# Kernel tuning notes

Measured on AMD Instinct MI355X. Metric: run time of the kernel, lower is better.

The kernel has to match this reference:

```python
import jax, jax.numpy as jnp
import numpy as np

EPS = 1e-5

def layer_norm(x, g, b):
    m = x.mean(-1, keepdims=True)
    v = ((x - m) ** 2).mean(-1, keepdims=True)
    return (x - m) * jax.lax.rsqrt(v + EPS) * g + b

def setup_inputs() -> dict:
    key = jax.random.key(0)
    ks = jax.random.split(key, 8)
    H, T = 512, 256
    hidden_states = jax.random.normal(ks[0], (1, T, H), jnp.float32)
    U = jax.random.normal(ks[1], (H, H), jnp.float32) * 0.01
    W = jax.random.normal(ks[2], (H, H), jnp.float32) * 0.01
    a = jax.random.normal(ks[3], (H,), jnp.float32) * 0.01
    b = jax.random.normal(ks[4], (H,), jnp.float32) * 0.01
    gamma = jnp.ones((H,), jnp.float32)
    beta = jnp.zeros((H,), jnp.float32)
    targets = jax.random.randint(ks[5], (T,), 0, H)  # deterministic stand-in for torch.randint dummy targets
    return {"hidden_states": hidden_states, "U": U, "W": W, "a": a, "b": b,
            "gamma": gamma, "beta": beta, "targets": targets}

def reference(hidden_states, U, W, a, b, gamma, beta, targets):
    # batch must be 1 (torch.outer in the original requires 1-D vectors)
    h = hidden_states[0]                      # (T, H)
    z = jax.nn.relu(h @ U + a)                # (T, H) slow-path hidden

    # Per-timestep grads of CE(LayerNorm(z_t @ W + b), target_t) w.r.t. W, b
    def step_loss(z_t, tgt, W_, b_):
        y = layer_norm(z_t @ W_ + b_, gamma, beta)
        return -jax.nn.log_softmax(y)[tgt]
    grad_fn = jax.grad(step_loss, argnums=(2, 3))
    gradW, gradb = jax.vmap(grad_fn, in_axes=(0, 0, None, None))(z, targets, W, b)  # (T,H,H), (T,H)

    # W_update_t[p,q] = sum_{i<t} h_i[p] * h_t[q] * gradW_i[p,q]
    G = h[:, :, None] * gradW                 # (T, H, H)
    A = jnp.cumsum(G, axis=0) - G             # exclusive prefix sum over i
    W_upd = A * h[:, None, :]                 # (T, H, H)
    fastW = W - jnp.cumsum(W_upd, axis=0)     # cumulative fast weights per t

    # b_update_t[q] = h_t[q] * sum_{i<t} (sum_p h_i[p]) * gradb_i[q]
    c = h.sum(-1)                             # (T,)
    Bc = c[:, None] * gradb                   # (T, H)
    Bex = jnp.cumsum(Bc, axis=0) - Bc         # exclusive
    b_upd = h * Bex
    fastb = b - jnp.cumsum(b_upd, axis=0)     # (T, H)

    pre = jnp.einsum('th,thq->tq', z, fastW) + fastb
    out = layer_norm(pre, gamma, beta)        # (T, H)
    return out[None]                          # (1, T, H)
```

## Files before the change

### kernel.cpp

```cpp
#include <hip/hip_runtime.h>

#define T 256
#define H 512
#define EPSF 1e-5f

__device__ __forceinline__ float block_sum(float v, float* s4) {
    for (int o = 32; o; o >>= 1) v += __shfl_xor(v, o);
    int w = threadIdx.x >> 6;
    __syncthreads();
    if ((threadIdx.x & 63) == 0) s4[w] = v;
    __syncthreads();
    return s4[0] + s4[1] + s4[2] + s4[3];
}

__device__ __forceinline__ float block_max(float v, float* s4) {
    for (int o = 32; o; o >>= 1) v = fmaxf(v, __shfl_xor(v, o));
    int w = threadIdx.x >> 6;
    __syncthreads();
    if ((threadIdx.x & 63) == 0) s4[w] = v;
    __syncthreads();
    return fmaxf(fmaxf(s4[0], s4[1]), fmaxf(s4[2], s4[3]));
}

__global__ __launch_bounds__(256) void k1(
        const float* __restrict__ h, const float* __restrict__ U,
        const float* __restrict__ a, float* __restrict__ Z,
        float* __restrict__ HZ, float* __restrict__ c, float* __restrict__ S) {
    int bid = blockIdx.x, tid = threadIdx.x;
    int lane = tid & 63, w = tid >> 6;
    if (bid < 8) {
        __shared__ float csum[4][64];
        int q = bid * 64 + lane;
        int tbase = w * 64;
        float s = 0.f;
        for (int j = 0; j < 64; j += 8) {
            float v[8];
            #pragma unroll
            for (int u = 0; u < 8; ++u) v[u] = h[(tbase + j + u) * H + q];
            #pragma unroll
            for (int u = 0; u < 8; ++u) s += v[u];
        }
        csum[w][lane] = s;
        __syncthreads();
        float acc = 0.f;
        #pragma unroll
        for (int w2 = 0; w2 < 3; ++w2) if (w2 < w) acc += csum[w2][lane];
        for (int j = 0; j < 64; j += 8) {
            float v[8];
            #pragma unroll
            for (int u = 0; u < 8; ++u) v[u] = h[(tbase + j + u) * H + q];
            #pragma unroll
            for (int u = 0; u < 8; ++u) { acc += v[u]; S[(tbase + j + u) * H + q] = acc; }
        }
        return;
    }
    int b = bid - 8;
    int t0 = (b >> 2) * 2, qt = b & 3;
    __shared__ __align__(16) float sh[1024];
    __shared__ float2 part[3][2][64];
    ((float4*)sh)[tid] = ((const float4*)(h + t0 * H))[tid];
    __syncthreads();

    if (qt == 0 && w < 2) {
        float s = 0.f;
        #pragma unroll
        for (int j = 0; j < 8; ++j) s += sh[w * 512 + lane + j * 64];
        for (int o = 32; o; o >>= 1) s += __shfl_xor(s, o);
        if (lane == 0) c[t0 + w] = s;
    }

    int qc = qt * 64 + lane;
    const float2* U2 = (const float2*)U;
    float2 acc0 = {0.f, 0.f}, acc1 = {0.f, 0.f};
    int kbeg = w * 128;
    for (int k0 = kbeg; k0 < kbeg + 128; k0 += 8) {
        float2 bv[8];
        #pragma unroll
        for (int u = 0; u < 8; ++u) bv[u] = U2[(k0 + u) * 256 + qc];
        float a0[8], a1[8];
        #pragma unroll
        for (int u = 0; u < 8; ++u) { a0[u] = sh[k0 + u]; a1[u] = sh[512 + k0 + u]; }
        #pragma unroll
        for (int u = 0; u < 8; ++u) {
            acc0.x += a0[u] * bv[u].x; acc0.y += a0[u] * bv[u].y;
            acc1.x += a1[u] * bv[u].x; acc1.y += a1[u] * bv[u].y;
        }
    }
    if (w) { part[w - 1][0][lane] = acc0; part[w - 1][1][lane] = acc1; }
    __syncthreads();
    if (w == 0) {
        #pragma unroll
        for (int p = 0; p < 3; ++p) {
            acc0.x += part[p][0][lane].x; acc0.y += part[p][0][lane].y;
            acc1.x += part[p][1][lane].x; acc1.y += part[p][1][lane].y;
        }
        float2 av = ((const float2*)a)[qc];
        float z0x = fmaxf(acc0.x + av.x, 0.f), z0y = fmaxf(acc0.y + av.y, 0.f);
        float z1x = fmaxf(acc1.x + av.x, 0.f), z1y = fmaxf(acc1.y + av.y, 0.f);
        float2 h0 = ((float2*)sh)[qc], h1 = ((float2*)sh)[256 + qc];
        ((float2*)Z)[t0 * 256 + qc]        = make_float2(z0x, z0y);
        ((float2*)Z)[(t0 + 1) * 256 + qc]  = make_float2(z1x, z1y);
        ((float2*)HZ)[t0 * 256 + qc]       = make_float2(h0.x * z0x, h0.y * z0y);
        ((float2*)HZ)[(t0 + 1) * 256 + qc] = make_float2(h1.x * z1x, h1.y * z1y);
    }
}

__global__ __launch_bounds__(256) void k2(
        const float* __restrict__ Z, const float* __restrict__ W,
        const float* __restrict__ bb, const float* __restrict__ HZ,
        const float* __restrict__ c, float* __restrict__ u0,
        float* __restrict__ Beta) {
    __shared__ __align__(16) float smem[2 * 8 * 516 + 256];
    int bid = blockIdx.x, tid = threadIdx.x;
    int lane = tid & 63, w = tid >> 6;
    if (bid < 512) {
        float* sh = smem;
        float2* part = (float2*)(smem + 1024);
        int t0 = (bid >> 2) * 2, qt = bid & 3;
        ((float4*)sh)[tid] = ((const float4*)(Z + t0 * H))[tid];
        __syncthreads();
        int qc = qt * 64 + lane;
        const float2* W2 = (const float2*)W;
        float2 acc0 = {0.f, 0.f}, acc1 = {0.f, 0.f};
        int kbeg = w * 128;
        for (int k0 = kbeg; k0 < kbeg + 128; k0 += 8) {
            float2 bv[8];
            #pragma unroll
            for (int u = 0; u < 8; ++u) bv[u] = W2[(k0 + u) * 256 + qc];
            float a0[8], a1[8];
            #pragma unroll
            for (int u = 0; u < 8; ++u) { a0[u] = sh[k0 + u]; a1[u] = sh[512 + k0 + u]; }
            #pragma unroll
            for (int u = 0; u < 8; ++u) {
                acc0.x += a0[u] * bv[u].x; acc0.y += a0[u] * bv[u].y;
                acc1.x += a1[u] * bv[u].x; acc1.y += a1[u] * bv[u].y;
            }
        }
        if (w) { part[((w - 1) * 2 + 0) * 64 + lane] = acc0; part[((w - 1) * 2 + 1) * 64 + lane] = acc1; }
        __syncthreads();
        if (w == 0) {
            #pragma unroll
            for (int p = 0; p < 3; ++p) {
                float2 p0 = part[(p * 2 + 0) * 64 + lane];
                float2 p1 = part[(p * 2 + 1) * 64 + lane];
                acc0.x += p0.x; acc0.y += p0.y;
                acc1.x += p1.x; acc1.y += p1.y;
            }
            float2 bv = ((const float2*)bb)[qc];
            ((float2*)u0)[t0 * 256 + qc]       = make_float2(acc0.x + bv.x, acc0.y + bv.y);
            ((float2*)u0)[(t0 + 1) * 256 + qc] = make_float2(acc1.x + bv.x, acc1.y + bv.y);
        }
    } else {
        int b = bid - 512;
        int ti = b >> 5, ii = b & 31;
        if (ii > ti) return;
        int t0 = ti * 8, i0 = ii * 8;
        float* Zs = smem;
        float* Hs = smem + 8 * 516;
        float* red = smem + 2 * 8 * 516;
        #pragma unroll
        for (int j = 0; j < 4; ++j) {
            int idx = tid + j * 256;
            int row = idx >> 7, col4 = idx & 127;
            float4 v = ((const float4*)(Z + (t0 + row) * H))[col4];
            *(float4*)&Zs[row * 516 + col4 * 4] = v;
            float4 g = ((const float4*)(HZ + (i0 + row) * H))[col4];
            *(float4*)&Hs[row * 516 + col4 * 4] = g;
        }
        __syncthreads();
        int ks = tid >> 6, r = (tid >> 3) & 7, ci = tid & 7;
        float acc = 0.f;
        int kb = ks * 128;
        #pragma unroll 4
        for (int k0 = kb; k0 < kb + 128; k0 += 8) {
            float4 z0 = *(float4*)&Zs[r * 516 + k0];
            float4 z1 = *(float4*)&Zs[r * 516 + k0 + 4];
            float4 h0 = *(float4*)&Hs[ci * 516 + k0];
            float4 h1 = *(float4*)&Hs[ci * 516 + k0 + 4];
            acc += z0.x * h0.x + z0.y * h0.y + z0.z * h0.z + z0.w * h0.w
                 + z1.x * h1.x + z1.y * h1.y + z1.z * h1.z + z1.w * h1.w;
        }
        red[ks * 64 + r * 8 + ci] = acc;
        __syncthreads();
        if (tid < 64) {
            int r2 = tid >> 3, c2 = tid & 7;
            float v = red[tid] + red[64 + tid] + red[128 + tid] + red[192 + tid];
            int t = t0 + r2, i = i0 + c2;
            Beta[t * 256 + i] = (i < t) ? v + c[i] : 0.f;
        }
    }
}

__global__ __launch_bounds__(256) void k3(
        const float* __restrict__ u0, const float* __restrict__ gamma,
        const float* __restrict__ beta, const int* __restrict__ targets,
        const float* __restrict__ S, float* __restrict__ D, float* __restrict__ SD) {
    __shared__ float s4[4];
    int t = blockIdx.x, tid = threadIdx.x;
    float2 uv = ((const float2*)u0)[t * 256 + tid];
    float2 gv = ((const float2*)gamma)[tid];
    float2 bv = ((const float2*)beta)[tid];

    float m = block_sum(uv.x + uv.y, s4) * (1.f / H);
    float d0 = uv.x - m, d1 = uv.y - m;
    float var = block_sum(d0 * d0 + d1 * d1, s4) * (1.f / H);
    float s = rsqrtf(var + EPSF);
    float xh0 = d0 * s, xh1 = d1 * s;
    float y0 = xh0 * gv.x + bv.x;
    float y1 = xh1 * gv.y + bv.y;

    float ymax = block_max(fmaxf(y0, y1), s4);
    float e0 = __expf(y0 - ymax), e1 = __expf(y1 - ymax);
    float Zs = block_sum(e0 + e1, s4);
    float invZ = 1.f / Zs;
    int tgt = targets[t];
    float g0 = e0 * invZ - (2 * tid == tgt ? 1.f : 0.f);
    float g1 = e1 * invZ - (2 * tid + 1 == tgt ? 1.f : 0.f);
    float gy0 = g0 * gv.x, gy1 = g1 * gv.y;

    float mgy = block_sum(gy0 + gy1, s4) * (1.f / H);
    float mgx = block_sum(gy0 * xh0 + gy1 * xh1, s4) * (1.f / H);

    float dd0 = s * (gy0 - mgy - xh0 * mgx);
    float dd1 = s * (gy1 - mgy - xh1 * mgx);
    float2 sv = ((const float2*)S)[t * 256 + tid];
    ((float2*)D)[t * 256 + tid]  = make_float2(dd0, dd1);
    ((float2*)SD)[t * 256 + tid] = make_float2(sv.x * dd0, sv.y * dd1);
}

__global__ __launch_bounds__(256) void k5(
        const float* __restrict__ Beta, const float* __restrict__ D,
        const float* __restrict__ SD, float* __restrict__ A1p,
        float* __restrict__ A2p) {
    __shared__ float Brow[64];
    int bid = blockIdx.x, tid = threadIdx.x;
    int t = bid >> 2, kq = bid & 3;
    int qc = tid;
    int ibeg = kq * 64;
    int iend = min((t + 7) & ~7, ibeg + 64);
    float2 a1 = {0.f, 0.f}, a2 = {0.f, 0.f};
    if (ibeg < iend) {
        if (tid < 64) Brow[tid] = Beta[t * 256 + ibeg + tid];
        __syncthreads();
        const float2* D2 = (const float2*)D;
        const float2* SD2 = (const float2*)SD;
        for (int k0 = ibeg; k0 < iend; k0 += 8) {
            float2 dv[8], sv[8];
            #pragma unroll
            for (int u = 0; u < 8; ++u) {
                dv[u] = D2[(k0 + u) * 256 + qc];
                sv[u] = SD2[(k0 + u) * 256 + qc];
            }
            #pragma unroll
            for (int u = 0; u < 8; ++u) {
                float bw = Brow[k0 - ibeg + u];
                a1.x += bw * dv[u].x; a1.y += bw * dv[u].y;
                a2.x += bw * sv[u].x; a2.y += bw * sv[u].y;
            }
        }
    }
    ((float2*)A1p)[(kq * T + t) * 256 + qc] = a1;
    ((float2*)A2p)[(kq * T + t) * 256 + qc] = a2;
}

__global__ __launch_bounds__(256) void k6(
        const float* __restrict__ A1p, const float* __restrict__ A2p,
        const float* __restrict__ u0, const float* __restrict__ S,
        const float* __restrict__ gamma, const float* __restrict__ beta,
        float* __restrict__ out) {
    __shared__ float s4[4];
    int t = blockIdx.x, tid = threadIdx.x, qc = tid;
    float2 a1 = {0.f, 0.f}, a2 = {0.f, 0.f};
    #pragma unroll
    for (int sgs = 0; sgs < 4; ++sgs) {
        float2 v1 = ((const float2*)A1p)[(sgs * T + t) * 256 + qc];
        float2 v2 = ((const float2*)A2p)[(sgs * T + t) * 256 + qc];
        a1.x += v1.x; a1.y += v1.y;
        a2.x += v2.x; a2.y += v2.y;
    }
    float2 uv = ((const float2*)u0)[t * 256 + qc];
    float2 st = ((const float2*)S)[t * 256 + qc];
    float p0 = uv.x - st.x * a1.x + a2.x;
    float p1 = uv.y - st.y * a1.y + a2.y;
    float m = block_sum(p0 + p1, s4) * (1.f / H);
    float d0 = p0 - m, d1 = p1 - m;
    float var = block_sum(d0 * d0 + d1 * d1, s4) * (1.f / H);
    float s = rsqrtf(var + EPSF);
    float2 gv = ((const float2*)gamma)[qc];
    float2 bv = ((const float2*)beta)[qc];
    ((float2*)out)[t * 256 + qc] = make_float2(
        d0 * s * gv.x + bv.x, d1 * s * gv.y + bv.y);
}

extern "C" void kernel_launch(void* const* d_in, const int* in_sizes, int n_in,
                              void* d_out, int out_size, void* d_ws, size_t ws_size,
                              hipStream_t stream) {
    const float* h     = (const float*)d_in[0];
    const float* U     = (const float*)d_in[1];
    const float* W     = (const float*)d_in[2];
    const float* a     = (const float*)d_in[3];
    const float* b     = (const float*)d_in[4];
    const float* gamma = (const float*)d_in[5];
    const float* beta  = (const float*)d_in[6];
    const int*   tgt   = (const int*)d_in[7];
    float* out = (float*)d_out;

    float* ws = (float*)d_ws;
    float* Z    = ws;
    float* HZ   = Z    + T * H;
    float* u0   = HZ   + T * H;
    float* D    = u0   + T * H;
    float* SD   = D    + T * H;
    float* S    = SD   + T * H;
    float* A1p  = S    + T * H;
    float* A2p  = A1p  + 4 * T * H;
    float* c    = A2p  + 4 * T * H;
    float* Beta = c    + T;

    k1<<<520,  256, 0, stream>>>(h, U, a, Z, HZ, c, S);
    k2<<<1536, 256, 0, stream>>>(Z, W, b, HZ, c, u0, Beta);
    k3<<<T,    256, 0, stream>>>(u0, gamma, beta, tgt, S, D, SD);
    k5<<<4 * T, 256, 0, stream>>>(Beta, D, SD, A1p, A2p);
    k6<<<T,    256, 0, stream>>>(A1p, A2p, u0, S, gamma, beta, out);
}
```

Before: 115.6 us.

## Fuse prefix-reduction and final layernorm kernels; compact triangular grid in k2

Merges the k5 partial accumulation and the k6 layernorm into one 1024-thread block per timestep. The four i-groups now reduce through shared memory instead of writing A1p/A2p partials to global memory and reading them back in a separate launch. k2's lower-triangular tile launch is also compacted: block index maps to (ti, ii) through an inverse triangular-number computation, so no blocks launch only to exit immediately. This removes one kernel launch, the partial-buffer traffic, and the idle blocks, at the cost of larger blocks with lower occupancy per CU and a small sqrt-based index computation.

```diff
diff --git a/kernel.cpp b/kernel.cpp
--- a/kernel.cpp
+++ b/kernel.cpp
@@ -20,6 +20,18 @@
     if ((threadIdx.x & 63) == 0) s4[w] = v;
     __syncthreads();
     return fmaxf(fmaxf(s4[0], s4[1]), fmaxf(s4[2], s4[3]));
+}
+
+__device__ __forceinline__ float bsum16(float v, float* s16) {
+    for (int o = 32; o; o >>= 1) v += __shfl_xor(v, o);
+    int w = threadIdx.x >> 6;
+    __syncthreads();
+    if ((threadIdx.x & 63) == 0) s16[w] = v;
+    __syncthreads();
+    float r = 0.f;
+    #pragma unroll
+    for (int i = 0; i < 16; ++i) r += s16[i];
+    return r;
 }
 
 __global__ __launch_bounds__(256) void k1(
@@ -151,9 +163,11 @@
             ((float2*)u0)[(t0 + 1) * 256 + qc] = make_float2(acc1.x + bv.x, acc1.y + bv.y);
         }
     } else {
-        int b = bid - 512;
-        int ti = b >> 5, ii = b & 31;
-        if (ii > ti) return;
+        int e = bid - 512;
+        int ti = (int)((sqrtf(8.f * (float)e + 1.f) - 1.f) * 0.5f);
+        while ((ti + 1) * (ti + 2) / 2 <= e) ++ti;
+        while (ti * (ti + 1) / 2 > e) --ti;
+        int ii = e - ti * (ti + 1) / 2;
         int t0 = ti * 8, i0 = ii * 8;
         float* Zs = smem;
         float* Hs = smem + 8 * 516;
@@ -228,68 +242,55 @@
     ((float2*)SD)[t * 256 + tid] = make_float2(sv.x * dd0, sv.y * dd1);
 }
 
-__global__ __launch_bounds__(256) void k5(
+__global__ __launch_bounds__(1024) void k4(
         const float* __restrict__ Beta, const float* __restrict__ D,
-        const float* __restrict__ SD, float* __restrict__ A1p,
-        float* __restrict__ A2p) {
-    __shared__ float Brow[64];
-    int bid = blockIdx.x, tid = threadIdx.x;
-    int t = bid >> 2, kq = bid & 3;
-    int qc = tid;
-    int ibeg = kq * 64;
+        const float* __restrict__ SD, const float* __restrict__ u0,
+        const float* __restrict__ S, const float* __restrict__ gamma,
+        const float* __restrict__ beta, float* __restrict__ out) {
+    __shared__ float Brow[256];
+    __shared__ float r1[4][512];
+    __shared__ float r2[4][512];
+    __shared__ float s16[16];
+    int t = blockIdx.x, tid = threadIdx.x;
+    if (tid < 256) Brow[tid] = Beta[t * 256 + tid];
+    __syncthreads();
+
+    int ig = tid >> 8, qc = tid & 255;
+    int ibeg = ig * 64;
     int iend = min((t + 7) & ~7, ibeg + 64);
     float2 a1 = {0.f, 0.f}, a2 = {0.f, 0.f};
-    if (ibeg < iend) {
-        if (tid < 64) Brow[tid] = Beta[t * 256 + ibeg + tid];
-        __syncthreads();
-        const float2* D2 = (const float2*)D;
-        const float2* SD2 = (const float2*)SD;
-        for (int k0 = ibeg; k0 < iend; k0 += 8) {
-            float2 dv[8], sv[8];
-            #pragma unroll
-            for (int u = 0; u < 8; ++u) {
-                dv[u] = D2[(k0 + u) * 256 + qc];
-                sv[u] = SD2[(k0 + u) * 256 + qc];
-            }
-            #pragma unroll
-            for (int u = 0; u < 8; ++u) {
-                float bw = Brow[k0 - ibeg + u];
-                a1.x += bw * dv[u].x; a1.y += bw * dv[u].y;
-                a2.x += bw * sv[u].x; a2.y += bw * sv[u].y;
-            }
-        }
-    }
-    ((float2*)A1p)[(kq * T + t) * 256 + qc] = a1;
-    ((float2*)A2p)[(kq * T + t) * 256 + qc] = a2;
-}
-
-__global__ __launch_bounds__(256) void k6(
-        const float* __restrict__ A1p, const float* __restrict__ A2p,
-        const float* __restrict__ u0, const float* __restrict__ S,
-        const float* __restrict__ gamma, const float* __restrict__ beta,
-        float* __restrict__ out) {
-    __shared__ float s4[4];
-    int t = blockIdx.x, tid = threadIdx.x, qc = tid;
-    float2 a1 = {0.f, 0.f}, a2 = {0.f, 0.f};
-    #pragma unroll
-    for (int sgs = 0; sgs < 4; ++sgs) {
-        float2 v1 = ((const float2*)A1p)[(sgs * T + t) * 256 + qc];
-        float2 v2 = ((const float2*)A2p)[(sgs * T + t) * 256 + qc];
-        a1.x += v1.x; a1.y += v1.y;
-        a2.x += v2.x; a2.y += v2.y;
-    }
-    float2 uv = ((const float2*)u0)[t * 256 + qc];
-    float2 st = ((const float2*)S)[t * 256 + qc];
-    float p0 = uv.x - st.x * a1.x + a2.x;
-    float p1 = uv.y - st.y * a1.y + a2.y;
-    float m = block_sum(p0 + p1, s4) * (1.f / H);
-    float d0 = p0 - m, d1 = p1 - m;
-    float var = block_sum(d0 * d0 + d1 * d1, s4) * (1.f / H);
+    const float2* D2 = (const float2*)D;
+    const float2* SD2 = (const float2*)SD;
+    for (int k0 = ibeg; k0 < iend; k0 += 8) {
+        float2 dv[8], sv[8];
+        #pragma unroll
+        for (int u = 0; u < 8; ++u) {
+            dv[u] = D2[(k0 + u) * 256 + qc];
+            sv[u] = SD2[(k0 + u) * 256 + qc];
+        }
+        #pragma unroll
+        for (int u = 0; u < 8; ++u) {
+            float bw = Brow[k0 + u];
+            a1.x += bw * dv[u].x; a1.y += bw * dv[u].y;
+            a2.x += bw * sv[u].x; a2.y += bw * sv[u].y;
+        }
+    }
+    r1[ig][2 * qc] = a1.x; r1[ig][2 * qc + 1] = a1.y;
+    r2[ig][2 * qc] = a2.x; r2[ig][2 * qc + 1] = a2.y;
+    __syncthreads();
+
+    float p = 0.f;
+    if (tid < 512) {
+        float A1 = r1[0][tid] + r1[1][tid] + r1[2][tid] + r1[3][tid];
+        float A2 = r2[0][tid] + r2[1][tid] + r2[2][tid] + r2[3][tid];
+        p = u0[t * H + tid] - S[t * H + tid] * A1 + A2;
+    }
+    float m = bsum16(p, s16) * (1.f / H);
+    float d = (tid < 512) ? p - m : 0.f;
+    float var = bsum16(d * d, s16) * (1.f / H);
     float s = rsqrtf(var + EPSF);
-    float2 gv = ((const float2*)gamma)[qc];
-    float2 bv = ((const float2*)beta)[qc];
-    ((float2*)out)[t * 256 + qc] = make_float2(
-        d0 * s * gv.x + bv.x, d1 * s * gv.y + bv.y);
+    if (tid < 512)
+        out[t * H + tid] = d * s * gamma[tid] + beta[tid];
 }
 
 extern "C" void kernel_launch(void* const* d_in, const int* in_sizes, int n_in,
@@ -306,20 +307,18 @@
     float* out = (float*)d_out;
 
     float* ws = (float*)d_ws;
+    const int TH = T * H;
     float* Z    = ws;
-    float* HZ   = Z    + T * H;
-    float* u0   = HZ   + T * H;
-    float* D    = u0   + T * H;
-    float* SD   = D    + T * H;
-    float* S    = SD   + T * H;
-    float* A1p  = S    + T * H;
-    float* A2p  = A1p  + 4 * T * H;
-    float* c    = A2p  + 4 * T * H;
+    float* HZ   = Z    + TH;
+    float* u0   = HZ   + TH;
+    float* D    = u0   + TH;
+    float* SD   = D    + TH;
+    float* S    = SD   + TH;
+    float* c    = S    + TH;
     float* Beta = c    + T;
 
     k1<<<520,  256, 0, stream>>>(h, U, a, Z, HZ, c, S);
-    k2<<<1536, 256, 0, stream>>>(Z, W, b, HZ, c, u0, Beta);
+    k2<<<1040, 256, 0, stream>>>(Z, W, b, HZ, c, u0, Beta);
     k3<<<T,    256, 0, stream>>>(u0, gamma, beta, tgt, S, D, SD);
-    k5<<<4 * T, 256, 0, stream>>>(Beta, D, SD, A1p, A2p);
-    k6<<<T,    256, 0, stream>>>(A1p, A2p, u0, S, gamma, beta, out);
-}
+    k4<<<T,   1024, 0, stream>>>(Beta, D, SD, u0, S, gamma, beta, out);
+}
```

Result: no change. 113.4 us, median of 2 (-1.9%).
